# Kernel optimization log

Measured on AMD Instinct MI355X. Metric: run time of the kernel, lower is better.

The kernel has to match this reference:

```python
import jax, jax.numpy as jnp
import numpy as np

B, T, D, H = 8, 4096, 512, 512


def log_g(x):
    # log of g(x) where g(x) = relu(x) + 0.5 for x >= 0, sigmoid(x) for x < 0
    return jnp.where(x >= 0, jnp.log(jax.nn.relu(x) + 0.5), -jax.nn.softplus(-x))


def setup_inputs() -> dict:
    key = jax.random.key(0)
    kx, kh0, kwz, kbz, kwh, kbh = jax.random.split(key, 6)
    s = 1.0 / np.sqrt(D)
    return {
        "x": jax.random.normal(kx, (B, T, D), dtype=jnp.float32),
        "h_0": jax.random.uniform(kh0, (B, H), dtype=jnp.float32),
        "Wz": jax.random.uniform(kwz, (H, D), dtype=jnp.float32, minval=-s, maxval=s),
        "bz": jax.random.uniform(kbz, (H,), dtype=jnp.float32, minval=-s, maxval=s),
        "Wh": jax.random.uniform(kwh, (H, D), dtype=jnp.float32, minval=-s, maxval=s),
        "bh": jax.random.uniform(kbh, (H,), dtype=jnp.float32, minval=-s, maxval=s),
    }


def parallel_scan_log(log_coeffs, log_values):
    # log_coeffs: (B, T, H), log_values: (B, T+1, H)
    a_star = jnp.cumsum(jnp.pad(log_coeffs, ((0, 0), (1, 0), (0, 0))), axis=1)  # (B, T+1, H)
    log_h = a_star + jax.lax.cumlogsumexp(log_values - a_star, axis=1)
    return jnp.exp(log_h)  # (B, T+1, H)


def reference(x, h_0, Wz, bz, Wh, bh):
    k = jnp.einsum('btd,hd->bth', x, Wz) + bz                # (B, T, H)
    log_z = -jax.nn.softplus(-k)                              # log sigmoid(k)
    log_coeffs = -jax.nn.softplus(k)                          # log (1 - sigmoid(k))
    log_h0 = log_g(h_0)[:, None, :]                           # (B, 1, H)
    log_tilde_h = log_g(jnp.einsum('btd,hd->bth', x, Wh) + bh)
    vals = jnp.concatenate([log_h0, log_z + log_tilde_h], axis=1)  # (B, T+1, H)
    h = parallel_scan_log(log_coeffs, vals)
    return h[:, -x.shape[1]:, :]                              # (B, T, H)
```

## Files before the change

### kernel.cpp

```cpp
#include <hip/hip_runtime.h>
#include <math.h>

#define Bq 8
#define Tq 4096
#define Dq 512
#define Hq 512
#define Mq (Bq * Tq)
#define NC 64
#define CL 64

typedef unsigned short ushort_t;
typedef unsigned int uint_t;
typedef __bf16 bf16x8 __attribute__((ext_vector_type(8)));
typedef float f32x4 __attribute__((ext_vector_type(4)));

__device__ __forceinline__ ushort_t f2bf(float f) {
    unsigned int u = __float_as_uint(f);
    unsigned int r = u + 0x7fffu + ((u >> 16) & 1u);
    return (ushort_t)(r >> 16);
}

__device__ __forceinline__ void gload16(const void* g, void* l) {
    __builtin_amdgcn_global_load_lds(
        (const __attribute__((address_space(1))) void*)g,
        (__attribute__((address_space(3))) void*)l, 16, 0, 0);
}

__device__ __forceinline__ void gates(uint_t w, float& c, float& v) {
    float k  = __uint_as_float((w & 0xffffu) << 16);
    float th = __uint_as_float(w & 0xffff0000u);
    float ek = __expf(k);
    c = 1.0f / (1.0f + ek);
    float z = 1.0f - c;
    float g = (th >= 0.0f) ? (th + 0.5f) : (1.0f / (1.0f + __expf(-th)));
    v = z * g;
}

__global__ __launch_bounds__(256)
void convert_all(const float* __restrict__ x, const float* __restrict__ Wz,
                 const float* __restrict__ Wh, ushort_t* __restrict__ dst) {
    size_t i8 = ((size_t)blockIdx.x * 256 + threadIdx.x) * 8;
    const size_t XN = (size_t)Mq * Dq;
    const size_t WN = (size_t)Hq * Dq;
    const float* src; size_t off;
    if (i8 < XN)            { src = x;  off = i8; }
    else if (i8 < XN + WN)  { src = Wz; off = i8 - XN; }
    else                    { src = Wh; off = i8 - XN - WN; }
    float4 a = *reinterpret_cast<const float4*>(src + off);
    float4 b = *reinterpret_cast<const float4*>(src + off + 4);
    uint4 o;
    o.x = (uint_t)f2bf(a.x) | ((uint_t)f2bf(a.y) << 16);
    o.y = (uint_t)f2bf(a.z) | ((uint_t)f2bf(a.w) << 16);
    o.z = (uint_t)f2bf(b.x) | ((uint_t)f2bf(b.y) << 16);
    o.w = (uint_t)f2bf(b.z) | ((uint_t)f2bf(b.w) << 16);
    *reinterpret_cast<uint4*>(dst + i8) = o;
}

__global__ __launch_bounds__(256, 2)
void gemm_fused(const ushort_t* __restrict__ xb, const ushort_t* __restrict__ wb,
                const float* __restrict__ bz, const float* __restrict__ bh,
                uint_t* __restrict__ kvout, float2* __restrict__ chAW) {
    __shared__ __align__(16) ushort_t smem[3 * 128 * 64];
    ushort_t* As  = smem;
    ushort_t* Bzs = smem + 128 * 64;
    ushort_t* Bhs = smem + 2 * 128 * 64;

    const int tid  = threadIdx.x;
    const int lane = tid & 63;
    const int wave = tid >> 6;
    const int wm = (wave >> 1) * 64;
    const int wn = (wave & 1) * 64;
    const int mBase = blockIdx.x * 128;
    const int nBase = blockIdx.y * 128;
    const ushort_t* Wzb = wb;
    const ushort_t* Whb = wb + (size_t)Hq * Dq;

    f32x4 zero = {0.f, 0.f, 0.f, 0.f};
    f32x4 accz[4][4], acch[4][4];
#pragma unroll
    for (int i = 0; i < 4; ++i)
#pragma unroll
        for (int j = 0; j < 4; ++j) { accz[i][j] = zero; acch[i][j] = zero; }

    const int rowInW = lane >> 3;
    const int ccG = (lane & 7) ^ rowInW;
    const int swz = lane & 7;

    for (int k0 = 0; k0 < Dq; k0 += 64) {
#pragma unroll
        for (int j = 0; j < 4; ++j) {
            const int rseg = j * 4 + wave;
            const int row  = rseg * 8 + rowInW;
            const size_t gcol = (size_t)(k0 + ccG * 8);
            gload16(xb  + (size_t)(mBase + row) * Dq + gcol, &As [rseg * 512]);
            gload16(Wzb + (size_t)(nBase + row) * Dq + gcol, &Bzs[rseg * 512]);
            gload16(Whb + (size_t)(nBase + row) * Dq + gcol, &Bhs[rseg * 512]);
        }
        __syncthreads();

#pragma unroll
        for (int ks = 0; ks < 2; ++ks) {
            const int cc = ks * 4 + (lane >> 4);
            const int sc = cc ^ swz;
            bf16x8 af[4], bzf[4], bhf[4];
#pragma unroll
            for (int i = 0; i < 4; ++i) {
                int rowA = wm + i * 16 + (lane & 15);
                af[i] = *reinterpret_cast<const bf16x8*>(&As[rowA * 64 + sc * 8]);
            }
#pragma unroll
            for (int i = 0; i < 4; ++i) {
                int rowB = wn + i * 16 + (lane & 15);
                bzf[i] = *reinterpret_cast<const bf16x8*>(&Bzs[rowB * 64 + sc * 8]);
                bhf[i] = *reinterpret_cast<const bf16x8*>(&Bhs[rowB * 64 + sc * 8]);
            }
#pragma unroll
            for (int mi = 0; mi < 4; ++mi)
#pragma unroll
                for (int ni = 0; ni < 4; ++ni) {
                    accz[mi][ni] = __builtin_amdgcn_mfma_f32_16x16x32_bf16(
                        af[mi], bzf[ni], accz[mi][ni], 0, 0, 0);
                    acch[mi][ni] = __builtin_amdgcn_mfma_f32_16x16x32_bf16(
                        af[mi], bhf[ni], acch[mi][ni], 0, 0, 0);
                }
        }
        __syncthreads();
    }

    const int colL = lane & 15;
    const int quad = lane >> 4;
    float2* sb = reinterpret_cast<float2*>(smem) + wave * 1024;

#pragma unroll
    for (int ni = 0; ni < 4; ++ni) {
        int h = nBase + wn + ni * 16 + colL;
        float bzv = bz[h];
        float bhv = bh[h];
#pragma unroll
        for (int mi = 0; mi < 4; ++mi) {
            float A = 1.f, W = 0.f;
#pragma unroll
            for (int r = 0; r < 4; ++r) {
                int bt = mBase + wm + mi * 16 + quad * 4 + r;
                float kf  = accz[mi][ni][r] + bzv;
                float thf = acch[mi][ni][r] + bhv;
                uint_t word = (uint_t)f2bf(kf) | ((uint_t)f2bf(thf) << 16);
                kvout[(size_t)bt * Hq + h] = word;
                float c, v;
                gates(word, c, v);
                W = fmaf(c, W, v);
                A *= c;
            }
            sb[(mi * 4 + quad) * 64 + ni * 16 + colL] = make_float2(A, W);
        }
    }
    __syncthreads();
    {
        float A = 1.f, W = 0.f;
#pragma unroll
        for (int s = 0; s < 16; ++s) {
            float2 aw = sb[s * 64 + lane];
            W = fmaf(aw.x, W, aw.y);
            A *= aw.x;
        }
        int g = blockIdx.x * 2 + (wm >> 6);
        int h = nBase + wn + lane;
        chAW[(size_t)g * Hq + h] = make_float2(A, W);
    }
}

__global__ __launch_bounds__(512)
void scan_final(const uint_t* kv, const float* __restrict__ h0,
                const float2* __restrict__ chAW, float* out) {
    const int b = blockIdx.x & 7;
    const int chunk = 63 - (blockIdx.x >> 3);
    const int h = threadIdx.x;

    float x0 = h0[(size_t)b * Hq + h];
    float r = (x0 >= 0.f) ? (x0 + 0.5f) : (1.f / (1.f + __expf(-x0)));

    const float2* p = chAW + (size_t)b * NC * Hq + h;
    int j = 0;
    for (; j + 8 <= chunk; j += 8) {
        float2 aw[8];
#pragma unroll
        for (int q = 0; q < 8; ++q) aw[q] = p[(size_t)(j + q) * Hq];
#pragma unroll
        for (int q = 0; q < 8; ++q) r = fmaf(aw[q].x, r, aw[q].y);
    }
    for (; j < chunk; ++j) {
        float2 aw = p[(size_t)j * Hq];
        r = fmaf(aw.x, r, aw.y);
    }

    const size_t base = ((size_t)b * Tq + (size_t)chunk * CL) * Hq + h;
    const uint_t* kvp = kv + base;
    float* op = out + base;

    uint_t w[16];
#pragma unroll
    for (int q = 0; q < 16; ++q) w[q] = kvp[(size_t)q * Hq];
    for (int bt = 0; bt < 4; ++bt) {
        uint_t wn[16];
        if (bt < 3) {
#pragma unroll
            for (int q = 0; q < 16; ++q)
                wn[q] = kvp[(size_t)((bt + 1) * 16 + q) * Hq];
        }
#pragma unroll
        for (int q = 0; q < 16; ++q) {
            float c, v;
            gates(w[q], c, v);
            r = fmaf(c, r, v);
            op[(size_t)(bt * 16 + q) * Hq] = r;
        }
#pragma unroll
        for (int q = 0; q < 16; ++q) w[q] = wn[q];
    }
}

extern "C" void kernel_launch(void* const* d_in, const int* in_sizes, int n_in,
                              void* d_out, int out_size, void* d_ws, size_t ws_size,
                              hipStream_t stream) {
    const float* x  = (const float*)d_in[0];
    const float* h0 = (const float*)d_in[1];
    const float* Wz = (const float*)d_in[2];
    const float* bz = (const float*)d_in[3];
    const float* Wh = (const float*)d_in[4];
    const float* bh = (const float*)d_in[5];
    float* out = (float*)d_out;

    char* ws = (char*)d_ws;
    ushort_t* xb = (ushort_t*)ws;
    ushort_t* wb = xb + (size_t)Mq * Dq;
    float2* chAW = (float2*)(wb + 2 * (size_t)Hq * Dq);
    uint_t* kv = (uint_t*)d_out;

    const int totalConv = (Mq * Dq + 2 * Hq * Dq) / (256 * 8);
    convert_all<<<dim3(totalConv), dim3(256), 0, stream>>>(x, Wz, Wh, xb);
    gemm_fused<<<dim3(Mq / 128, Hq / 128), dim3(256), 0, stream>>>(xb, wb, bz, bh, kv, chAW);
    scan_final<<<dim3(Bq * NC), dim3(512), 0, stream>>>(kv, h0, chAW, out);
}
```

Baseline: 197.3 us.

## Triple-buffer GEMM K-loop with BK=32 and async LDS prefetch two tiles ahead

Replaces the single-buffered 64-wide K-step loop, which synchronized twice per iteration, with a three-stage ring of 32-wide K tiles. Tiles are loaded two steps ahead with global_load_lds, and partial vmcnt waits plus one barrier per step let the loads overlap the MFMA work. The LDS swizzle is redone for the narrower tile. The risks are a larger LDS footprint that may lower occupancy, tricky hand-written waitcnt and barrier correctness, and the epilogue reusing smem right after a bare barrier.

```diff
diff --git a/kernel.cpp b/kernel.cpp
--- a/kernel.cpp
+++ b/kernel.cpp
@@ -8,6 +8,8 @@
 #define Mq (Bq * Tq)
 #define NC 64
 #define CL 64
+#define BK 32
+#define NKT (Dq / BK)
 
 typedef unsigned short ushort_t;
 typedef unsigned int uint_t;
@@ -60,10 +62,7 @@
 void gemm_fused(const ushort_t* __restrict__ xb, const ushort_t* __restrict__ wb,
                 const float* __restrict__ bz, const float* __restrict__ bh,
                 uint_t* __restrict__ kvout, float2* __restrict__ chAW) {
-    __shared__ __align__(16) ushort_t smem[3 * 128 * 64];
-    ushort_t* As  = smem;
-    ushort_t* Bzs = smem + 128 * 64;
-    ushort_t* Bhs = smem + 2 * 128 * 64;
+    __shared__ __align__(16) ushort_t smem[3 * 3 * 128 * BK];
 
     const int tid  = threadIdx.x;
     const int lane = tid & 63;
@@ -82,50 +81,72 @@
 #pragma unroll
         for (int j = 0; j < 4; ++j) { accz[i][j] = zero; acch[i][j] = zero; }
 
-    const int rowInW = lane >> 3;
-    const int ccG = (lane & 7) ^ rowInW;
-    const int swz = lane & 7;
-
-    for (int k0 = 0; k0 < Dq; k0 += 64) {
-#pragma unroll
-        for (int j = 0; j < 4; ++j) {
-            const int rseg = j * 4 + wave;
-            const int row  = rseg * 8 + rowInW;
-            const size_t gcol = (size_t)(k0 + ccG * 8);
-            gload16(xb  + (size_t)(mBase + row) * Dq + gcol, &As [rseg * 512]);
-            gload16(Wzb + (size_t)(nBase + row) * Dq + gcol, &Bzs[rseg * 512]);
-            gload16(Whb + (size_t)(nBase + row) * Dq + gcol, &Bhs[rseg * 512]);
-        }
-        __syncthreads();
-
-#pragma unroll
-        for (int ks = 0; ks < 2; ++ks) {
-            const int cc = ks * 4 + (lane >> 4);
-            const int sc = cc ^ swz;
-            bf16x8 af[4], bzf[4], bhf[4];
-#pragma unroll
-            for (int i = 0; i < 4; ++i) {
-                int rowA = wm + i * 16 + (lane & 15);
-                af[i] = *reinterpret_cast<const bf16x8*>(&As[rowA * 64 + sc * 8]);
+    const int srowL = lane >> 2;
+    const int spc   = lane & 3;
+
+    ushort_t* const b0 = smem;
+    ushort_t* const b1 = smem + 3 * 128 * BK;
+    ushort_t* const b2 = smem + 6 * 128 * BK;
+    ushort_t* bufs[3] = {b0, b1, b2};
+
+    auto STAGE = [&](int t, ushort_t* buf) {
+        const int k0 = t * BK;
+#pragma unroll
+        for (int j = 0; j < 2; ++j) {
+            const int r   = wave * 2 + j;
+            const int row = r * 16 + srowL;
+            const int lc  = spc ^ ((row >> 1) & 3);
+            const size_t gcol = (size_t)(k0 + lc * 8);
+            ushort_t* ldst = buf + r * 512;
+            gload16(xb  + (size_t)(mBase + row) * Dq + gcol, ldst);
+            gload16(Wzb + (size_t)(nBase + row) * Dq + gcol, ldst + 128 * BK);
+            gload16(Whb + (size_t)(nBase + row) * Dq + gcol, ldst + 2 * 128 * BK);
+        }
+    };
+
+    STAGE(0, b0);
+    STAGE(1, b1);
+    asm volatile("s_waitcnt vmcnt(6)" ::: "memory");
+    __builtin_amdgcn_s_barrier();
+
+    const int rl15 = lane & 15;
+    const int cc   = lane >> 4;
+
+#pragma unroll
+    for (int t = 0; t < NKT; ++t) {
+        const ushort_t* A   = bufs[t % 3];
+        const ushort_t* Bzs = A + 128 * BK;
+        const ushort_t* Bhs = A + 2 * 128 * BK;
+        bf16x8 af[4], bzf[4], bhf[4];
+#pragma unroll
+        for (int i = 0; i < 4; ++i) {
+            const int rowA = wm + i * 16 + rl15;
+            const int pA   = cc ^ ((rowA >> 1) & 3);
+            af[i] = *reinterpret_cast<const bf16x8*>(A + rowA * BK + pA * 8);
+            const int rowB = wn + i * 16 + rl15;
+            const int pB   = cc ^ ((rowB >> 1) & 3);
+            bzf[i] = *reinterpret_cast<const bf16x8*>(Bzs + rowB * BK + pB * 8);
+            bhf[i] = *reinterpret_cast<const bf16x8*>(Bhs + rowB * BK + pB * 8);
+        }
+        if (t + 2 < NKT) STAGE(t + 2, bufs[(t + 2) % 3]);
+#pragma unroll
+        for (int mi = 0; mi < 4; ++mi)
+#pragma unroll
+            for (int ni = 0; ni < 4; ++ni) {
+                accz[mi][ni] = __builtin_amdgcn_mfma_f32_16x16x32_bf16(
+                    af[mi], bzf[ni], accz[mi][ni], 0, 0, 0);
+                acch[mi][ni] = __builtin_amdgcn_mfma_f32_16x16x32_bf16(
+                    af[mi], bhf[ni], acch[mi][ni], 0, 0, 0);
             }
-#pragma unroll
-            for (int i = 0; i < 4; ++i) {
-                int rowB = wn + i * 16 + (lane & 15);
-                bzf[i] = *reinterpret_cast<const bf16x8*>(&Bzs[rowB * 64 + sc * 8]);
-                bhf[i] = *reinterpret_cast<const bf16x8*>(&Bhs[rowB * 64 + sc * 8]);
-            }
-#pragma unroll
-            for (int mi = 0; mi < 4; ++mi)
-#pragma unroll
-                for (int ni = 0; ni < 4; ++ni) {
-                    accz[mi][ni] = __builtin_amdgcn_mfma_f32_16x16x32_bf16(
-                        af[mi], bzf[ni], accz[mi][ni], 0, 0, 0);
-                    acch[mi][ni] = __builtin_amdgcn_mfma_f32_16x16x32_bf16(
-                        af[mi], bhf[ni], acch[mi][ni], 0, 0, 0);
-                }
-        }
-        __syncthreads();
-    }
+        if (t < NKT - 2) {
+            asm volatile("s_waitcnt vmcnt(6)" ::: "memory");
+            __builtin_amdgcn_s_barrier();
+        } else if (t < NKT - 1) {
+            asm volatile("s_waitcnt vmcnt(0)" ::: "memory");
+            __builtin_amdgcn_s_barrier();
+        }
+    }
+    __builtin_amdgcn_s_barrier();
 
     const int colL = lane & 15;
     const int quad = lane >> 4;
```

Measured after the change: 196.0 us. No clear change (-0.7%).
